# Performance work log

Hardware: AMD Instinct MI355X
Metric: run time of the kernel (lower is better)

Reference implementation:

```python
import jax, jax.numpy as jnp
import numpy as np

NEG_SLOPE = 0.01  # torch LeakyReLU default
BN_EPS = 1e-5     # torch BatchNorm1d default


def _bn(x, g, b):
    # training-mode batch norm over the node axis
    m = jnp.mean(x, axis=0)
    v = jnp.var(x, axis=0)
    return g * (x - m) * jax.lax.rsqrt(v + BN_EPS) + b


def _lrelu(x):
    return jax.nn.leaky_relu(x, NEG_SLOPE)


def setup_inputs() -> dict:
    key = jax.random.key(0)
    N, E, W, D = 100_000, 1_600_000, 32, 10
    ks = iter(jax.random.split(key, 64))

    def w(shape):
        fan_in = shape[-2] if len(shape) >= 2 else shape[-1]
        return (jax.random.normal(next(ks), shape, jnp.float32) / np.sqrt(fan_in)).astype(jnp.float32)

    inp = {}
    inp["x"] = jax.random.normal(next(ks), (N, 1), jnp.float32)
    inp["col_e_idx"] = jax.random.randint(next(ks), (2, E), 0, N, dtype=jnp.int32)
    # init_node_feature_trans: MLP 1 -> [32] -> 32, LeakyReLU, batch_norm=True
    inp["Wi0"] = w((1, W)); inp["bi0"] = jnp.zeros(W); inp["gi0"] = jnp.ones(W); inp["bei0"] = jnp.zeros(W)
    inp["Wi1"] = w((W, W)); inp["bi1"] = jnp.zeros(W); inp["gi1"] = jnp.ones(W); inp["bei1"] = jnp.zeros(W)
    # 10 CollConv layers (identical dims -> stacked params)
    inp["Wm"] = w((D, W, W)); inp["bm"] = jnp.zeros((D, W)); inp["gm"] = jnp.ones((D, W)); inp["bem"] = jnp.zeros((D, W))
    inp["Wu"] = w((D, 2 * W, W)); inp["bu"] = jnp.zeros((D, W)); inp["gu"] = jnp.ones((D, W)); inp["beu"] = jnp.zeros((D, W))
    # final_mlp: 32 -> 256 -> 128 -> 64 -> 32 (LeakyReLU, no BN), then 32 -> 1 sigmoid
    inp["Wf0"] = w((W, 256)); inp["bf0"] = jnp.zeros(256)
    inp["Wf1"] = w((256, 128)); inp["bf1"] = jnp.zeros(128)
    inp["Wf2"] = w((128, 64)); inp["bf2"] = jnp.zeros(64)
    inp["Wf3"] = w((64, W)); inp["bf3"] = jnp.zeros(W)
    inp["Wo"] = w((W, 1)); inp["bo"] = jnp.zeros(1)
    return inp


def reference(x, col_e_idx, Wi0, bi0, gi0, bei0, Wi1, bi1, gi1, bei1,
              Wm, bm, gm, bem, Wu, bu, gu, beu,
              Wf0, bf0, Wf1, bf1, Wf2, bf2, Wf3, bf3, Wo, bo):
    N = x.shape[0]
    D = Wm.shape[0]
    src, dst = col_e_idx[0], col_e_idx[1]

    # init node-feature MLP (Linear -> BN -> LeakyReLU, twice)
    h = _lrelu(_bn(x @ Wi0 + bi0, gi0, bei0))
    h = _lrelu(_bn(h @ Wi1 + bi1, gi1, bei1))

    feats = [h]  # middle_features[0]
    for i in range(D):  # fixed small depth -> python loop is fine
        # CollConv: node-wise message transform, edge gather, scatter-sum, update
        msg = _lrelu(_bn(h @ Wm[i] + bm[i], gm[i], bem[i]))      # [N, W]
        agg = jax.ops.segment_sum(msg[src], dst, num_segments=N)  # [N, W]
        h = _lrelu(_bn(jnp.concatenate([h, agg], axis=-1) @ Wu[i] + bu[i], gu[i], beu[i]))
        if i - 2 >= 0:  # residual_skip_num = 2
            h = h + feats[i - 2]
        feats.append(h)

    # final MLP (no BN) + sigmoid head
    h = _lrelu(h @ Wf0 + bf0)
    h = _lrelu(h @ Wf1 + bf1)
    h = _lrelu(h @ Wf2 + bf2)
    h = _lrelu(h @ Wf3 + bf3)
    return jax.nn.sigmoid(h @ Wo + bo)  # [N, 1]
```

## Files before the change

### kernel.cpp

```cpp
#include <hip/hip_runtime.h>
#include <hip/hip_bf16.h>

#define NN 100000
#define NEDGE 1600000
#define NV (NN*32)
#define NEG 0.01f
#define EPS 1e-5f
#define NBLK 391
#define NBKT 391
#define CHUNK 4096
#define NCBLK 391
#define DCAP 6144
#define STC 64
#define ST_STRIDE 4096
#define NGBLK 1563

#define OFF_STATS 0
#define STATS_F  (22*ST_STRIDE)
#define OFF_PA   STATS_F
#define OFF_PB   (OFF_PA + NV)
#define OFF_AGG  (OFF_PB + NV)
#define OFF_MSGB (OFF_AGG + NV)
#define OFF_RING (OFF_MSGB + NV/2)
#define OFF_WF   (OFF_RING + 4*NV)
#define ARENA_F  (OFF_WF + 25600)

#define W0B 0
#define W1B 1024
#define W2B 5120
#define W3B 6144

__device__ __align__(16) float gA[ARENA_F];
__device__ int g_rowptr[NN + 1];
__device__ int g_csr[NEDGE];
__device__ int g_bin[NEDGE];
__device__ int g_bcnt[NBKT];
__device__ int g_boff[NBKT];
__device__ int g_btail[NBKT];

__device__ __forceinline__ float lrelu(float v) { return v > 0.f ? v : v * NEG; }
__device__ __forceinline__ unsigned short f2b(float v) {
    __hip_bfloat16 b = __float2bfloat16(v);
    return *reinterpret_cast<unsigned short*>(&b);
}
__device__ __forceinline__ float b2f(unsigned short u) {
    __hip_bfloat16 b = *reinterpret_cast<__hip_bfloat16*>(&u);
    return __bfloat162float(b);
}

__global__ void k_zero_v19()
{
    int i = blockIdx.x * 256 + threadIdx.x;
    if (i < STATS_F) gA[i] = 0.f;
    if (i < NBKT) g_bcnt[i] = 0;
}

__global__ __launch_bounds__(256) void k_bcnt_v19(const int* __restrict__ col)
{
    __shared__ int hist[NBKT];
    int tid = threadIdx.x;
    for (int b = tid; b < NBKT; b += 256) hist[b] = 0;
    __syncthreads();
    int e0 = blockIdx.x * CHUNK;
    #pragma unroll
    for (int r = 0; r < CHUNK / 256; ++r) {
        int e = e0 + r * 256 + tid;
        if (e < NEDGE) atomicAdd(&hist[col[NEDGE + e] >> 8], 1);
    }
    __syncthreads();
    for (int b = tid; b < NBKT; b += 256) {
        int v = hist[b];
        if (v) atomicAdd(&g_bcnt[b], v);
    }
}

__global__ __launch_bounds__(512) void k_bscan_v19()
{
    __shared__ int s[512];
    int t = threadIdx.x;
    int v = (t < NBKT) ? g_bcnt[t] : 0;
    s[t] = v;
    __syncthreads();
    for (int off = 1; off < 512; off <<= 1) {
        int u = (t >= off) ? s[t - off] : 0;
        __syncthreads();
        s[t] += u;
        __syncthreads();
    }
    if (t < NBKT) {
        int o = s[t] - v;
        g_boff[t] = o;
        g_btail[t] = o;
    }
}

__global__ __launch_bounds__(256) void k_binfill_v19(const int* __restrict__ col)
{
    __shared__ int ssrc[CHUNK];
    __shared__ int sdst[CHUNK];
    __shared__ int hist[NBKT];
    __shared__ int boffL[NBKT];
    __shared__ int cnt2[NBKT];
    int tid = threadIdx.x;
    for (int b = tid; b < NBKT; b += 256) { hist[b] = 0; cnt2[b] = 0; }
    __syncthreads();
    int e0 = blockIdx.x * CHUNK;
    #pragma unroll
    for (int r = 0; r < CHUNK / 256; ++r) {
        int i = r * 256 + tid;
        int e = e0 + i;
        if (e < NEDGE) {
            int s = col[e];
            int d = col[NEDGE + e];
            ssrc[i] = s;
            sdst[i] = d;
            atomicAdd(&hist[d >> 8], 1);
        }
    }
    __syncthreads();
    for (int b = tid; b < NBKT; b += 256) {
        int h = hist[b];
        if (h) boffL[b] = atomicAdd(&g_btail[b], h);
    }
    __syncthreads();
    #pragma unroll
    for (int r = 0; r < CHUNK / 256; ++r) {
        int i = r * 256 + tid;
        int e = e0 + i;
        if (e < NEDGE) {
            int d = sdst[i];
            int b = d >> 8;
            int rk = atomicAdd(&cnt2[b], 1);
            g_bin[boffL[b] + rk] = (ssrc[i] << 8) | (d & 255);
        }
    }
}

__global__ __launch_bounds__(256) void k_csr_v19()
{
    __shared__ int stg[DCAP];
    __shared__ int c1[256];
    __shared__ int sc[256];
    __shared__ int sl[256];
    __shared__ int c2[256];
    int tid = threadIdx.x, b = blockIdx.x;
    int base = g_boff[b];
    int cntE = g_bcnt[b];
    c1[tid] = 0; c2[tid] = 0;
    __syncthreads();
    for (int i = tid; i < cntE; i += 256) {
        int p = g_bin[base + i];
        if (i < DCAP) stg[i] = p;
        atomicAdd(&c1[p & 255], 1);
    }
    __syncthreads();
    int v = c1[tid];
    sc[tid] = v;
    __syncthreads();
    for (int off = 1; off < 256; off <<= 1) {
        int u = (tid >= off) ? sc[tid - off] : 0;
        __syncthreads();
        sc[tid] += u;
        __syncthreads();
    }
    int loff = sc[tid] - v;
    sl[tid] = loff;
    int node = b * 256 + tid;
    if (node < NN) g_rowptr[node] = base + loff;
    if (b == NBKT - 1 && tid == 0) g_rowptr[NN] = NEDGE;
    __syncthreads();
    for (int i = tid; i < cntE; i += 256) {
        int p = (i < DCAP) ? stg[i] : g_bin[base + i];
        int dl = p & 255;
        int rk = atomicAdd(&c2[dl], 1);
        g_csr[base + sl[dl] + rk] = p >> 8;
    }
}

__global__ void k_init0_v17(const float* __restrict__ x, const float* __restrict__ Wi0,
                            const float* __restrict__ bi0)
{
    int j = threadIdx.x & 31, ns = threadIdx.x >> 5;
    float w = Wi0[j];
    float bb = bi0[j];
    __shared__ float red[64];
    if (threadIdx.x < 64) red[threadIdx.x] = 0.f;
    __syncthreads();
    float s1 = 0.f, s2 = 0.f;
    for (int t = blockIdx.x; t < NN / 8; t += gridDim.x) {
        int n = t * 8 + ns;
        float v = x[n] * w + bb;
        gA[OFF_PA + n * 32 + j] = v;
        s1 += v; s2 += v * v;
    }
    atomicAdd(&red[j], s1);
    atomicAdd(&red[j + 32], s2);
    __syncthreads();
    if (threadIdx.x < 64)
        atomicAdd(&gA[OFF_STATS + (blockIdx.x & (STC - 1)) * 64 + threadIdx.x], red[threadIdx.x]);
}

__global__ void k_nl_v17(int off_in, int off_out, int out_msg, int st_in,
                         const float* __restrict__ gamma, const float* __restrict__ beta,
                         int off_resid, int off_feats,
                         const float* __restrict__ Wn, const float* __restrict__ bn,
                         int st_out)
{
    int j = threadIdx.x & 31, ns = threadIdx.x >> 5;
    __shared__ float sstat[64];
    __shared__ float red[64];
    if (threadIdx.x < 64) {
        red[threadIdx.x] = 0.f;
        float acc = 0.f;
        int base = st_in + threadIdx.x;
        #pragma unroll 8
        for (int c = 0; c < STC; ++c) acc += gA[base + c * 64];
        sstat[threadIdx.x] = acc;
    }
    __syncthreads();
    float mean = sstat[j] * (1.f / NN);
    float var  = sstat[32 + j] * (1.f / NN) - mean * mean;
    float scale = gamma[j] * rsqrtf(var + EPS);
    float shift = beta[j] - mean * scale;

    float wc[32]; float bb = 0.f;
    if (Wn) {
        #pragma unroll
        for (int k = 0; k < 32; ++k) wc[k] = Wn[k * 32 + j];
        bb = bn[j];
    }
    unsigned short* mb = (unsigned short*)(gA + OFF_MSGB);
    __shared__ float sH[8][32];
    float s1 = 0.f, s2 = 0.f;
    for (int t = blockIdx.x; t < NN / 8; t += gridDim.x) {
        int n = t * 8 + ns;
        float v = gA[off_in + n * 32 + j];
        v = lrelu(scale * v + shift);
        if (off_resid >= 0) v += gA[off_resid + n * 32 + j];
        if (off_feats >= 0) gA[off_feats + n * 32 + j] = v;
        if (Wn) {
            sH[ns][j] = v;
            __syncthreads();
            float acc = bb;
            #pragma unroll
            for (int k = 0; k < 32; k += 4) {
                float4 h4 = *(const float4*)&sH[ns][k];
                acc += h4.x * wc[k] + h4.y * wc[k + 1] + h4.z * wc[k + 2] + h4.w * wc[k + 3];
            }
            if (out_msg) mb[n * 32 + j] = f2b(acc);
            else gA[off_out + n * 32 + j] = acc;
            s1 += acc; s2 += acc * acc;
            __syncthreads();
        }
    }
    if (Wn) {
        atomicAdd(&red[j], s1);
        atomicAdd(&red[j + 32], s2);
        __syncthreads();
        if (threadIdx.x < 64)
            atomicAdd(&gA[st_out + (blockIdx.x & (STC - 1)) * 64 + threadIdx.x], red[threadIdx.x]);
    }
}

__global__ __launch_bounds__(256) void k_gupd_v20(int st_msg,
                                                  const float* __restrict__ gm,
                                                  const float* __restrict__ bem,
                                                  int off_h,
                                                  const float* __restrict__ Wu_i,
                                                  const float* __restrict__ bu_i,
                                                  int st_out)
{
    __shared__ float sstat[64];
    __shared__ float scl[32], shf[32];
    __shared__ float sH[64][36];
    __shared__ float sAgg[64][36];
    __shared__ float red[64];
    int tid = threadIdx.x;
    int nb = blockIdx.x * 64;

    if (tid < 64) {
        red[tid] = 0.f;
        float acc = 0.f;
        int base = st_msg + tid;
        #pragma unroll 8
        for (int c = 0; c < STC; ++c) acc += gA[base + c * 64];
        sstat[tid] = acc;
    }
    {
        const float* hp = gA + off_h + nb * 32;
        int lim = min(2048, (NN - nb) * 32);
        for (int idx = tid; idx < lim; idx += 256)
            sH[idx >> 5][idx & 31] = hp[idx];
    }
    __syncthreads();
    if (tid < 32) {
        float mean = sstat[tid] * (1.f / NN);
        float var  = sstat[32 + tid] * (1.f / NN) - mean * mean;
        float s = gm[tid] * rsqrtf(var + EPS);
        scl[tid] = s;
        shf[tid] = bem[tid] - mean * s;
    }
    __syncthreads();

    {
        int nl = tid >> 2;
        int g  = tid & 3;
        int n  = nb + nl;
        float c[8], h[8];
        #pragma unroll
        for (int q = 0; q < 8; ++q) { c[q] = scl[g * 8 + q]; h[q] = shf[g * 8 + q]; }
        float a[8];
        #pragma unroll
        for (int q = 0; q < 8; ++q) a[q] = 0.f;
        if (n < NN) {
            const unsigned short* mb = (const unsigned short*)(gA + OFF_MSGB);
            int e0 = g_rowptr[n], e1 = g_rowptr[n + 1];
            int e = e0;
            for (; e + 3 < e1; e += 4) {
                int s0 = g_csr[e];
                int s1 = g_csr[e + 1];
                int s2 = g_csr[e + 2];
                int s3 = g_csr[e + 3];
                uint4 m0 = *(const uint4*)(mb + (s0 << 5) + (g << 3));
                uint4 m1 = *(const uint4*)(mb + (s1 << 5) + (g << 3));
                uint4 m2 = *(const uint4*)(mb + (s2 << 5) + (g << 3));
                uint4 m3 = *(const uint4*)(mb + (s3 << 5) + (g << 3));
                #pragma unroll
                for (int w = 0; w < 4; ++w) {
                    unsigned int u0 = (&m0.x)[w], u1 = (&m1.x)[w], u2 = (&m2.x)[w], u3 = (&m3.x)[w];
                    int q = w * 2;
                    a[q]   += lrelu(c[q]   * b2f((unsigned short)(u0 & 0xffff)) + h[q])
                            + lrelu(c[q]   * b2f((unsigned short)(u1 & 0xffff)) + h[q])
                            + lrelu(c[q]   * b2f((unsigned short)(u2 & 0xffff)) + h[q])
                            + lrelu(c[q]   * b2f((unsigned short)(u3 & 0xffff)) + h[q]);
                    a[q+1] += lrelu(c[q+1] * b2f((unsigned short)(u0 >> 16)) + h[q+1])
                            + lrelu(c[q+1] * b2f((unsigned short)(u1 >> 16)) + h[q+1])
                            + lrelu(c[q+1] * b2f((unsigned short)(u2 >> 16)) + h[q+1])
                            + lrelu(c[q+1] * b2f((unsigned short)(u3 >> 16)) + h[q+1]);
                }
            }
            for (; e < e1; ++e) {
                int s0 = g_csr[e];
                uint4 m0 = *(const uint4*)(mb + (s0 << 5) + (g << 3));
                #pragma unroll
                for (int w = 0; w < 4; ++w) {
                    unsigned int u0 = (&m0.x)[w];
                    int q = w * 2;
                    a[q]   += lrelu(c[q]   * b2f((unsigned short)(u0 & 0xffff)) + h[q]);
                    a[q+1] += lrelu(c[q+1] * b2f((unsigned short)(u0 >> 16)) + h[q+1]);
                }
            }
        }
        *(float4*)&sAgg[nl][g * 8]     = make_float4(a[0], a[1], a[2], a[3]);
        *(float4*)&sAgg[nl][g * 8 + 4] = make_float4(a[4], a[5], a[6], a[7]);
    }
    __syncthreads();

    {
        int j = tid & 31, ns = tid >> 5;
        float wc[64];
        #pragma unroll
        for (int k = 0; k < 64; ++k) wc[k] = Wu_i[k * 32 + j];
        float bb = bu_i[j];
        float s1 = 0.f, s2 = 0.f;
        #pragma unroll
        for (int it = 0; it < 8; ++it) {
            int nl = it * 8 + ns;
            int n = nb + nl;
            if (n >= NN) break;
            float acc = bb;
            #pragma unroll
            for (int k = 0; k < 32; k += 4) {
                float4 h4 = *(const float4*)&sH[nl][k];
                acc += h4.x * wc[k] + h4.y * wc[k + 1] + h4.z * wc[k + 2] + h4.w * wc[k + 3];
                float4 a4 = *(const float4*)&sAgg[nl][k];
                acc += a4.x * wc[32 + k] + a4.y * wc[32 + k + 1] + a4.z * wc[32 + k + 2] + a4.w * wc[32 + k + 3];
            }
            gA[OFF_PB + n * 32 + j] = acc;
            s1 += acc; s2 += acc * acc;
        }
        atomicAdd(&red[j], s1);
        atomicAdd(&red[j + 32], s2);
        __syncthreads();
        if (tid < 64)
            atomicAdd(&gA[st_out + (blockIdx.x & (STC - 1)) * 64 + tid], red[tid]);
    }
}

typedef __attribute__((ext_vector_type(8))) short bf16x8;
typedef __attribute__((ext_vector_type(4))) float f32x4;

union FC { uint4 u; bf16x8 b; };

#define MFMA(a, b, c) __builtin_amdgcn_mfma_f32_16x16x32_bf16(a, b, c, 0, 0, 0)

__device__ __forceinline__ bf16x8 ld_wf(const uint4* p) {
    FC c; c.u = *p; return c.b;
}

__device__ __forceinline__ f32x4 ld_bias4(const float* p) {
    float4 t = *(const float4*)p;
    f32x4 r; r[0] = t.x; r[1] = t.y; r[2] = t.z; r[3] = t.w; return r;
}

__device__ __forceinline__ f32x4 lrelu4(f32x4 v) {
    f32x4 r;
    #pragma unroll
    for (int k = 0; k < 4; ++k) r[k] = v[k] > 0.f ? v[k] : v[k] * NEG;
    return r;
}

__device__ __forceinline__ void splitpack(const float* v, bf16x8& hi, bf16x8& lo) {
    unsigned int h[4], l[4];
    #pragma unroll
    for (int k = 0; k < 4; ++k) {
        unsigned short h0 = f2b(v[2*k]), h1 = f2b(v[2*k+1]);
        float r0 = v[2*k]   - b2f(h0);
        float r1 = v[2*k+1] - b2f(h1);
        h[k] = (unsigned int)h0 | ((unsigned int)h1 << 16);
        l[k] = (unsigned int)f2b(r0) | ((unsigned int)f2b(r1) << 16);
    }
    FC ch; ch.u = make_uint4(h[0], h[1], h[2], h[3]); hi = ch.b;
    FC cl; cl.u = make_uint4(l[0], l[1], l[2], l[3]); lo = cl.b;
}

__global__ __launch_bounds__(256) void k_wprep_v18(const float* __restrict__ W0,
                                                   const float* __restrict__ W1,
                                                   const float* __restrict__ W2,
                                                   const float* __restrict__ W3)
{
    int i = blockIdx.x * 256 + threadIdx.x;
    if (i >= 51200) return;
    const float* src; int Nout, nk; int r = i;
    if (r < 8192)       { src = W0; Nout = 256; nk = 1; }
    else if (r < 40960) { src = W1; Nout = 128; nk = 8; r -= 8192; }
    else if (r < 49152) { src = W2; Nout = 64;  nk = 4; r -= 40960; }
    else                { src = W3; Nout = 32;  nk = 2; r -= 49152; }
    int frag = r >> 9;
    int lane = (r >> 3) & 63;
    int j = r & 7;
    int T = frag / nk, s = frag - T * nk;
    int g = lane >> 4;
    int outf = T * 16 + (lane & 15);
    int inf = 32 * s + 16 * (j >> 2) + 4 * g + (j & 3);
    unsigned short* dst = (unsigned short*)(gA + OFF_WF);
    dst[i] = f2b(src[inf * Nout + outf]);
}

__global__ __launch_bounds__(256) void k_final_v18(
    int off_h,
    const float* __restrict__ bf0, const float* __restrict__ bf1,
    const float* __restrict__ bf2, const float* __restrict__ bf3,
    const float* __restrict__ Wo,  const float* __restrict__ bo,
    float* __restrict__ out)
{
    int lane = threadIdx.x & 63;
    int wave = threadIdx.x >> 6;
    int c = lane & 15;
    int g = lane >> 4;
    int nb = blockIdx.x * 128 + wave * 32;
    int n0 = nb + c;
    int n1 = nb + 16 + c;
    int ld0 = min(n0, NN - 1), ld1 = min(n1, NN - 1);

    const float* h = gA + off_h;
    const uint4* WF = (const uint4*)(gA + OFF_WF);

    float4 ia0 = *(const float4*)&h[ld0 * 32 + 4 * g];
    float4 ib0 = *(const float4*)&h[ld0 * 32 + 16 + 4 * g];
    float4 ia1 = *(const float4*)&h[ld1 * 32 + 4 * g];
    float4 ib1 = *(const float4*)&h[ld1 * 32 + 16 + 4 * g];
    bf16x8 Bh0, Bl0, Bh1, Bl1;
    {
        float v0[8] = {ia0.x, ia0.y, ia0.z, ia0.w, ib0.x, ib0.y, ib0.z, ib0.w};
        float v1[8] = {ia1.x, ia1.y, ia1.z, ia1.w, ib1.x, ib1.y, ib1.z, ib1.w};
        splitpack(v0, Bh0, Bl0);
        splitpack(v1, Bh1, Bl1);
    }

    f32x4 A0[16][2];
    #pragma unroll
    for (int t = 0; t < 16; ++t) {
        f32x4 ci = ld_bias4(bf0 + t * 16 + 4 * g);
        bf16x8 w = ld_wf(WF + W0B + t * 64 + lane);
        f32x4 d0 = MFMA(w, Bh0, ci);
        d0 = MFMA(w, Bl0, d0);
        f32x4 d1 = MFMA(w, Bh1, ci);
        d1 = MFMA(w, Bl1, d1);
        A0[t][0] = lrelu4(d0);
        A0[t][1] = lrelu4(d1);
    }

    f32x4 A1[8][2];
    #pragma unroll
    for (int T = 0; T < 8; ++T) {
        f32x4 ci = ld_bias4(bf1 + T * 16 + 4 * g);
        A1[T][0] = ci; A1[T][1] = ci;
    }
    #pragma unroll
    for (int s = 0; s < 8; ++s) {
        bf16x8 bh[2], bl[2];
        #pragma unroll
        for (int u = 0; u < 2; ++u) {
            float vv[8] = {A0[2*s][u][0], A0[2*s][u][1], A0[2*s][u][2], A0[2*s][u][3],
                           A0[2*s+1][u][0], A0[2*s+1][u][1], A0[2*s+1][u][2], A0[2*s+1][u][3]};
            splitpack(vv, bh[u], bl[u]);
        }
        #pragma unroll
        for (int T = 0; T < 8; ++T) {
            bf16x8 w = ld_wf(WF + W1B + (T * 8 + s) * 64 + lane);
            A1[T][0] = MFMA(w, bh[0], A1[T][0]);
            A1[T][0] = MFMA(w, bl[0], A1[T][0]);
            A1[T][1] = MFMA(w, bh[1], A1[T][1]);
            A1[T][1] = MFMA(w, bl[1], A1[T][1]);
        }
    }
    #pragma unroll
    for (int T = 0; T < 8; ++T) { A1[T][0] = lrelu4(A1[T][0]); A1[T][1] = lrelu4(A1[T][1]); }

    f32x4 A2[4][2];
    #pragma unroll
    for (int T = 0; T < 4; ++T) {
        f32x4 ci = ld_bias4(bf2 + T * 16 + 4 * g);
        A2[T][0] = ci; A2[T][1] = ci;
    }
    #pragma unroll
    for (int s = 0; s < 4; ++s) {
        bf16x8 bh[2], bl[2];
        #pragma unroll
        for (int u = 0; u < 2; ++u) {
            float vv[8] = {A1[2*s][u][0], A1[2*s][u][1], A1[2*s][u][2], A1[2*s][u][3],
                           A1[2*s+1][u][0], A1[2*s+1][u][1], A1[2*s+1][u][2], A1[2*s+1][u][3]};
            splitpack(vv, bh[u], bl[u]);
        }
        #pragma unroll
        for (int T = 0; T < 4; ++T) {
            bf16x8 w = ld_wf(WF + W2B + (T * 4 + s) * 64 + lane);
            A2[T][0] = MFMA(w, bh[0], A2[T][0]);
            A2[T][0] = MFMA(w, bl[0], A2[T][0]);
            A2[T][1] = MFMA(w, bh[1], A2[T][1]);
            A2[T][1] = MFMA(w, bl[1], A2[T][1]);
        }
    }
    #pragma unroll
    for (int T = 0; T < 4; ++T) { A2[T][0] = lrelu4(A2[T][0]); A2[T][1] = lrelu4(A2[T][1]); }

    f32x4 A3[2][2];
    #pragma unroll
    for (int T = 0; T < 2; ++T) {
        f32x4 ci = ld_bias4(bf3 + T * 16 + 4 * g);
        A3[T][0] = ci; A3[T][1] = ci;
    }
    #pragma unroll
    for (int s = 0; s < 2; ++s) {
        bf16x8 bh[2], bl[2];
        #pragma unroll
        for (int u = 0; u < 2; ++u) {
            float vv[8] = {A2[2*s][u][0], A2[2*s][u][1], A2[2*s][u][2], A2[2*s][u][3],
                           A2[2*s+1][u][0], A2[2*s+1][u][1], A2[2*s+1][u][2], A2[2*s+1][u][3]};
            splitpack(vv, bh[u], bl[u]);
        }
        #pragma unroll
        for (int T = 0; T < 2; ++T) {
            bf16x8 w = ld_wf(WF + W3B + (T * 2 + s) * 64 + lane);
            A3[T][0] = MFMA(w, bh[0], A3[T][0]);
            A3[T][0] = MFMA(w, bl[0], A3[T][0]);
            A3[T][1] = MFMA(w, bh[1], A3[T][1]);
            A3[T][1] = MFMA(w, bl[1], A3[T][1]);
        }
    }
    #pragma unroll
    for (int T = 0; T < 2; ++T) { A3[T][0] = lrelu4(A3[T][0]); A3[T][1] = lrelu4(A3[T][1]); }

    float4 woa = *(const float4*)&Wo[4 * g];
    float4 wob = *(const float4*)&Wo[16 + 4 * g];
    float z0 = A3[0][0][0]*woa.x + A3[0][0][1]*woa.y + A3[0][0][2]*woa.z + A3[0][0][3]*woa.w
             + A3[1][0][0]*wob.x + A3[1][0][1]*wob.y + A3[1][0][2]*wob.z + A3[1][0][3]*wob.w;
    float z1 = A3[0][1][0]*woa.x + A3[0][1][1]*woa.y + A3[0][1][2]*woa.z + A3[0][1][3]*woa.w
             + A3[1][1][0]*wob.x + A3[1][1][1]*wob.y + A3[1][1][2]*wob.z + A3[1][1][3]*wob.w;
    z0 += __shfl_xor(z0, 16); z0 += __shfl_xor(z0, 32);
    z1 += __shfl_xor(z1, 16); z1 += __shfl_xor(z1, 32);
    float bb = bo[0];
    if (g == 0 && n0 < NN) out[n0] = 1.f / (1.f + __expf(-(z0 + bb)));
    if (g == 1 && n1 < NN) out[n1] = 1.f / (1.f + __expf(-(z1 + bb)));
}

extern "C" void kernel_launch(void* const* d_in, const int* in_sizes, int n_in,
                              void* d_out, int out_size, void* d_ws, size_t ws_size,
                              hipStream_t stream)
{
    (void)in_sizes; (void)n_in; (void)out_size; (void)d_ws; (void)ws_size;
    float* out = (float*)d_out;

    const float* x   = (const float*)d_in[0];
    const int*  col  = (const int*) d_in[1];
    const float* Wi0 = (const float*)d_in[2];
    const float* bi0 = (const float*)d_in[3];
    const float* gi0 = (const float*)d_in[4];
    const float* bei0= (const float*)d_in[5];
    const float* Wi1 = (const float*)d_in[6];
    const float* bi1 = (const float*)d_in[7];
    const float* gi1 = (const float*)d_in[8];
    const float* bei1= (const float*)d_in[9];
    const float* Wm  = (const float*)d_in[10];
    const float* bm  = (const float*)d_in[11];
    const float* gm  = (const float*)d_in[12];
    const float* bem = (const float*)d_in[13];
    const float* Wu  = (const float*)d_in[14];
    const float* bu  = (const float*)d_in[15];
    const float* gu  = (const float*)d_in[16];
    const float* beu = (const float*)d_in[17];
    const float* Wf0 = (const float*)d_in[18];
    const float* bf0 = (const float*)d_in[19];
    const float* Wf1 = (const float*)d_in[20];
    const float* bf1 = (const float*)d_in[21];
    const float* Wf2 = (const float*)d_in[22];
    const float* bf2 = (const float*)d_in[23];
    const float* Wf3 = (const float*)d_in[24];
    const float* bf3 = (const float*)d_in[25];
    const float* Wo  = (const float*)d_in[26];
    const float* bo  = (const float*)d_in[27];

    const int st_i0 = OFF_STATS;
    const int st_i1 = OFF_STATS + ST_STRIDE;
    const int st_m  = OFF_STATS + 2 * ST_STRIDE;
    const int st_u  = OFF_STATS + 12 * ST_STRIDE;

    const int RING[4] = { OFF_RING, OFF_RING + NV, OFF_RING + 2 * NV, OFF_RING + 3 * NV };

    dim3 blk(256);
    k_zero_v19<<<NBLK, blk, 0, stream>>>();
    k_bcnt_v19<<<NCBLK, blk, 0, stream>>>(col);
    k_bscan_v19<<<1, 512, 0, stream>>>();
    k_binfill_v19<<<NCBLK, blk, 0, stream>>>(col);
    k_csr_v19<<<NBKT, blk, 0, stream>>>();
    k_wprep_v18<<<200, blk, 0, stream>>>(Wf0, Wf1, Wf2, Wf3);

    k_init0_v17<<<1024, blk, 0, stream>>>(x, Wi0, bi0);
    k_nl_v17<<<1024, blk, 0, stream>>>(OFF_PA, OFF_PB, 0, st_i0, gi0, bei0, -1, -1, Wi1, bi1, st_i1);
    k_nl_v17<<<1024, blk, 0, stream>>>(OFF_PB, 0, 1, st_i1, gi1, bei1, -1, RING[0], Wm, bm, st_m);

    for (int i = 0; i < 10; ++i) {
        int h_cur = RING[i & 3];
        int h_new = RING[(i + 1) & 3];
        int resid = (i >= 2) ? RING[(i - 2) & 3] : -1;
        k_gupd_v20<<<NGBLK, blk, 0, stream>>>(st_m + i * ST_STRIDE, gm + i * 32, bem + i * 32,
                                              h_cur, Wu + i * 2048, bu + i * 32,
                                              st_u + i * ST_STRIDE);
        const float* Wn = (i < 9) ? (Wm + (i + 1) * 1024) : nullptr;
        const float* bn = (i < 9) ? (bm + (i + 1) * 32) : nullptr;
        int st_next = (i < 9) ? (st_m + (i + 1) * ST_STRIDE) : 0;
        k_nl_v17<<<1024, blk, 0, stream>>>(OFF_PB, 0, 1, st_u + i * ST_STRIDE,
                                           gu + i * 32, beu + i * 32,
                                           resid, h_new, Wn, bn, st_next);
    }

    k_final_v18<<<782, blk, 0, stream>>>(RING[2], bf0, bf1, bf2, bf3, Wo, bo, out);
}
```

Before: 966.8 us.

## Precompute activated messages per node before gather and sort CSR neighbors

Moves the BatchNorm+LeakyReLU of messages out of the per-edge gather loop into a separate per-node pass that writes activated bf16 messages, so the edge loop only sums. This applies the activation once per node instead of once per edge, at the cost of an extra kernel launch and an extra read/write of the message buffer each layer. The CSR build now sorts source indices within each destination row to improve gather locality, and the gather loop loads four neighbor indices with one coalesced load and distributes them via shuffles. The activated message is now rounded to bf16 after activation, which changes rounding slightly.

```diff
diff --git a/kernel.cpp b/kernel.cpp
--- a/kernel.cpp
+++ b/kernel.cpp
@@ -19,8 +19,8 @@
 #define STATS_F  (22*ST_STRIDE)
 #define OFF_PA   STATS_F
 #define OFF_PB   (OFF_PA + NV)
-#define OFF_AGG  (OFF_PB + NV)
-#define OFF_MSGB (OFF_AGG + NV)
+#define OFF_TACT (OFF_PB + NV)
+#define OFF_MSGB (OFF_TACT + NV)
 #define OFF_RING (OFF_MSGB + NV/2)
 #define OFF_WF   (OFF_RING + 4*NV)
 #define ARENA_F  (OFF_WF + 25600)
@@ -136,9 +136,10 @@
     }
 }
 
-__global__ __launch_bounds__(256) void k_csr_v19()
+__global__ __launch_bounds__(256) void k_csr_v21()
 {
     __shared__ int stg[DCAP];
+    __shared__ int srt[DCAP];
     __shared__ int c1[256];
     __shared__ int sc[256];
     __shared__ int sl[256];
@@ -169,11 +170,32 @@
     if (node < NN) g_rowptr[node] = base + loff;
     if (b == NBKT - 1 && tid == 0) g_rowptr[NN] = NEDGE;
     __syncthreads();
-    for (int i = tid; i < cntE; i += 256) {
-        int p = (i < DCAP) ? stg[i] : g_bin[base + i];
-        int dl = p & 255;
-        int rk = atomicAdd(&c2[dl], 1);
-        g_csr[base + sl[dl] + rk] = p >> 8;
+    if (cntE <= DCAP) {
+        for (int i = tid; i < cntE; i += 256) {
+            int p = stg[i];
+            int dl = p & 255;
+            int rk = atomicAdd(&c2[dl], 1);
+            srt[sl[dl] + rk] = p;
+        }
+        __syncthreads();
+        int cnt = v;
+        int s0 = loff;
+        for (int i = 1; i < cnt; ++i) {
+            int key = srt[s0 + i];
+            int j = i - 1;
+            while (j >= 0 && srt[s0 + j] > key) { srt[s0 + j + 1] = srt[s0 + j]; --j; }
+            srt[s0 + j + 1] = key;
+        }
+        __syncthreads();
+        for (int i = tid; i < cntE; i += 256)
+            g_csr[base + i] = srt[i] >> 8;
+    } else {
+        for (int i = tid; i < cntE; i += 256) {
+            int p = (i < DCAP) ? stg[i] : g_bin[base + i];
+            int dl = p & 255;
+            int rk = atomicAdd(&c2[dl], 1);
+            g_csr[base + sl[dl] + rk] = p >> 8;
+        }
     }
 }
 
@@ -262,35 +284,19 @@
     }
 }
 
-__global__ __launch_bounds__(256) void k_gupd_v20(int st_msg,
-                                                  const float* __restrict__ gm,
-                                                  const float* __restrict__ bem,
-                                                  int off_h,
-                                                  const float* __restrict__ Wu_i,
-                                                  const float* __restrict__ bu_i,
-                                                  int st_out)
+__global__ __launch_bounds__(256) void k_act_v21(int st_msg,
+                                                 const float* __restrict__ gm,
+                                                 const float* __restrict__ bem)
 {
     __shared__ float sstat[64];
     __shared__ float scl[32], shf[32];
-    __shared__ float sH[64][36];
-    __shared__ float sAgg[64][36];
-    __shared__ float red[64];
     int tid = threadIdx.x;
-    int nb = blockIdx.x * 64;
-
     if (tid < 64) {
-        red[tid] = 0.f;
         float acc = 0.f;
         int base = st_msg + tid;
         #pragma unroll 8
         for (int c = 0; c < STC; ++c) acc += gA[base + c * 64];
         sstat[tid] = acc;
-    }
-    {
-        const float* hp = gA + off_h + nb * 32;
-        int lim = min(2048, (NN - nb) * 32);
-        for (int idx = tid; idx < lim; idx += 256)
-            sH[idx >> 5][idx & 31] = hp[idx];
     }
     __syncthreads();
     if (tid < 32) {
@@ -301,53 +307,83 @@
         shf[tid] = bem[tid] - mean * s;
     }
     __syncthreads();
+    int idx = blockIdx.x * 256 + tid;
+    if (idx >= NV / 8) return;
+    const uint4* src = (const uint4*)(gA + OFF_MSGB);
+    uint4* dst = (uint4*)(gA + OFF_TACT);
+    uint4 m = src[idx];
+    int fb = (idx & 3) * 8;
+    uint4 o;
+    #pragma unroll
+    for (int w = 0; w < 4; ++w) {
+        unsigned int u = (&m.x)[w];
+        int f0 = fb + 2 * w;
+        float vlo = lrelu(scl[f0]     * __uint_as_float(u << 16)         + shf[f0]);
+        float vhi = lrelu(scl[f0 + 1] * __uint_as_float(u & 0xffff0000u) + shf[f0 + 1]);
+        (&o.x)[w] = (unsigned int)f2b(vlo) | ((unsigned int)f2b(vhi) << 16);
+    }
+    dst[idx] = o;
+}
+
+__global__ __launch_bounds__(256) void k_gupd_v21(int off_h,
+                                                  const float* __restrict__ Wu_i,
+                                                  const float* __restrict__ bu_i,
+                                                  int st_out)
+{
+    __shared__ float sH[64][36];
+    __shared__ float sAgg[64][36];
+    __shared__ float red[64];
+    int tid = threadIdx.x;
+    int nb = blockIdx.x * 64;
+
+    if (tid < 64) red[tid] = 0.f;
+    {
+        const float* hp = gA + off_h + nb * 32;
+        int lim = min(2048, (NN - nb) * 32);
+        for (int idx = tid; idx < lim; idx += 256)
+            sH[idx >> 5][idx & 31] = hp[idx];
+    }
 
     {
         int nl = tid >> 2;
         int g  = tid & 3;
         int n  = nb + nl;
-        float c[8], h[8];
-        #pragma unroll
-        for (int q = 0; q < 8; ++q) { c[q] = scl[g * 8 + q]; h[q] = shf[g * 8 + q]; }
         float a[8];
         #pragma unroll
         for (int q = 0; q < 8; ++q) a[q] = 0.f;
         if (n < NN) {
-            const unsigned short* mb = (const unsigned short*)(gA + OFF_MSGB);
+            const unsigned short* tb = (const unsigned short*)(gA + OFF_TACT);
             int e0 = g_rowptr[n], e1 = g_rowptr[n + 1];
             int e = e0;
             for (; e + 3 < e1; e += 4) {
-                int s0 = g_csr[e];
-                int s1 = g_csr[e + 1];
-                int s2 = g_csr[e + 2];
-                int s3 = g_csr[e + 3];
-                uint4 m0 = *(const uint4*)(mb + (s0 << 5) + (g << 3));
-                uint4 m1 = *(const uint4*)(mb + (s1 << 5) + (g << 3));
-                uint4 m2 = *(const uint4*)(mb + (s2 << 5) + (g << 3));
-                uint4 m3 = *(const uint4*)(mb + (s3 << 5) + (g << 3));
+                int sg = g_csr[e + g];
+                int s0 = __shfl(sg, 0, 4);
+                int s1 = __shfl(sg, 1, 4);
+                int s2 = __shfl(sg, 2, 4);
+                int s3 = __shfl(sg, 3, 4);
+                uint4 m0 = *(const uint4*)(tb + (s0 << 5) + (g << 3));
+                uint4 m1 = *(const uint4*)(tb + (s1 << 5) + (g << 3));
+                uint4 m2 = *(const uint4*)(tb + (s2 << 5) + (g << 3));
+                uint4 m3 = *(const uint4*)(tb + (s3 << 5) + (g << 3));
                 #pragma unroll
                 for (int w = 0; w < 4; ++w) {
                     unsigned int u0 = (&m0.x)[w], u1 = (&m1.x)[w], u2 = (&m2.x)[w], u3 = (&m3.x)[w];
                     int q = w * 2;
-                    a[q]   += lrelu(c[q]   * b2f((unsigned short)(u0 & 0xffff)) + h[q])
-                            + lrelu(c[q]   * b2f((unsigned short)(u1 & 0xffff)) + h[q])
-                            + lrelu(c[q]   * b2f((unsigned short)(u2 & 0xffff)) + h[q])
-                            + lrelu(c[q]   * b2f((unsigned short)(u3 & 0xffff)) + h[q]);
-                    a[q+1] += lrelu(c[q+1] * b2f((unsigned short)(u0 >> 16)) + h[q+1])
-                            + lrelu(c[q+1] * b2f((unsigned short)(u1 >> 16)) + h[q+1])
-                            + lrelu(c[q+1] * b2f((unsigned short)(u2 >> 16)) + h[q+1])
-                            + lrelu(c[q+1] * b2f((unsigned short)(u3 >> 16)) + h[q+1]);
+                    a[q]   += __uint_as_float(u0 << 16) + __uint_as_float(u1 << 16)
+                            + __uint_as_float(u2 << 16) + __uint_as_float(u3 << 16);
+                    a[q+1] += __uint_as_float(u0 & 0xffff0000u) + __uint_as_float(u1 & 0xffff0000u)
+                            + __uint_as_float(u2 & 0xffff0000u) + __uint_as_float(u3 & 0xffff0000u);
                 }
             }
             for (; e < e1; ++e) {
                 int s0 = g_csr[e];
-                uint4 m0 = *(const uint4*)(mb + (s0 << 5) + (g << 3));
+                uint4 m0 = *(const uint4*)(tb + (s0 << 5) + (g << 3));
                 #pragma unroll
                 for (int w = 0; w < 4; ++w) {
                     unsigned int u0 = (&m0.x)[w];
                     int q = w * 2;
-                    a[q]   += lrelu(c[q]   * b2f((unsigned short)(u0 & 0xffff)) + h[q]);
-                    a[q+1] += lrelu(c[q+1] * b2f((unsigned short)(u0 >> 16)) + h[q+1]);
+                    a[q]   += __uint_as_float(u0 << 16);
+                    a[q+1] += __uint_as_float(u0 & 0xffff0000u);
                 }
             }
         }
@@ -633,7 +669,7 @@
     k_bcnt_v19<<<NCBLK, blk, 0, stream>>>(col);
     k_bscan_v19<<<1, 512, 0, stream>>>();
     k_binfill_v19<<<NCBLK, blk, 0, stream>>>(col);
-    k_csr_v19<<<NBKT, blk, 0, stream>>>();
+    k_csr_v21<<<NBKT, blk, 0, stream>>>();
     k_wprep_v18<<<200, blk, 0, stream>>>(Wf0, Wf1, Wf2, Wf3);
 
     k_init0_v17<<<1024, blk, 0, stream>>>(x, Wi0, bi0);
@@ -644,8 +680,8 @@
         int h_cur = RING[i & 3];
         int h_new = RING[(i + 1) & 3];
         int resid = (i >= 2) ? RING[(i - 2) & 3] : -1;
-        k_gupd_v20<<<NGBLK, blk, 0, stream>>>(st_m + i * ST_STRIDE, gm + i * 32, bem + i * 32,
-                                              h_cur, Wu + i * 2048, bu + i * 32,
+        k_act_v21<<<1563, blk, 0, stream>>>(st_m + i * ST_STRIDE, gm + i * 32, bem + i * 32);
+        k_gupd_v21<<<NGBLK, blk, 0, stream>>>(h_cur, Wu + i * 2048, bu + i * 32,
                                               st_u + i * ST_STRIDE);
         const float* Wn = (i < 9) ? (Wm + (i + 1) * 1024) : nullptr;
         const float* bn = (i < 9) ? (bm + (i + 1) * 32) : nullptr;
```

Result: slower. 988.6 us (+2.3%).

## Degree-sort nodes within buckets, sort CSR by source, unroll gather by eight

Applied to the files above, without the earlier changes.

In the CSR build, nodes within each 256-node bucket are sorted by in-degree into a permutation table, and each node's edges are ordered by coarse source range. The gather/update kernel then processes nodes in permuted order, so the lanes of a wave see similar degrees and their source reads are more localized. The gather loop is also unrolled to eight edges, and bf16 is converted with plain bit shifts. The risks are extra setup work, indirect node indexing, and non-contiguous h loads and output stores.

```diff
diff --git a/kernel.cpp b/kernel.cpp
--- a/kernel.cpp
+++ b/kernel.cpp
@@ -13,14 +13,13 @@
 #define DCAP 6144
 #define STC 64
 #define ST_STRIDE 4096
-#define NGBLK 1563
+#define NGBLK 1564
 
 #define OFF_STATS 0
 #define STATS_F  (22*ST_STRIDE)
 #define OFF_PA   STATS_F
 #define OFF_PB   (OFF_PA + NV)
-#define OFF_AGG  (OFF_PB + NV)
-#define OFF_MSGB (OFF_AGG + NV)
+#define OFF_MSGB (OFF_PB + NV)
 #define OFF_RING (OFF_MSGB + NV/2)
 #define OFF_WF   (OFF_RING + 4*NV)
 #define ARENA_F  (OFF_WF + 25600)
@@ -34,6 +33,7 @@
 __device__ int g_rowptr[NN + 1];
 __device__ int g_csr[NEDGE];
 __device__ int g_bin[NEDGE];
+__device__ int g_perm[NBKT * 256];
 __device__ int g_bcnt[NBKT];
 __device__ int g_boff[NBKT];
 __device__ int g_btail[NBKT];
@@ -136,26 +136,36 @@
     }
 }
 
-__global__ __launch_bounds__(256) void k_csr_v19()
+__global__ __launch_bounds__(256) void k_csr_v23()
 {
     __shared__ int stg[DCAP];
-    __shared__ int c1[256];
+    __shared__ int c1[1024];
+    __shared__ int sgb[1024];
+    __shared__ int c2[1024];
     __shared__ int sc[256];
     __shared__ int sl[256];
-    __shared__ int c2[256];
+    __shared__ int dh[256];
+    __shared__ int ds2[256];
     int tid = threadIdx.x, b = blockIdx.x;
     int base = g_boff[b];
     int cntE = g_bcnt[b];
-    c1[tid] = 0; c2[tid] = 0;
+    #pragma unroll
+    for (int k = 0; k < 4; ++k) { c1[tid + 256 * k] = 0; c2[tid + 256 * k] = 0; }
+    dh[tid] = 0;
     __syncthreads();
     for (int i = tid; i < cntE; i += 256) {
         int p = g_bin[base + i];
         if (i < DCAP) stg[i] = p;
-        atomicAdd(&c1[p & 255], 1);
-    }
-    __syncthreads();
-    int v = c1[tid];
-    sc[tid] = v;
+        atomicAdd(&c1[((p & 255) << 2) | (p >> 23)], 1);
+    }
+    __syncthreads();
+    int t0 = c1[tid * 4], t1 = c1[tid * 4 + 1], t2 = c1[tid * 4 + 2], t3 = c1[tid * 4 + 3];
+    int deg = t0 + t1 + t2 + t3;
+    sgb[tid * 4]     = 0;
+    sgb[tid * 4 + 1] = t0;
+    sgb[tid * 4 + 2] = t0 + t1;
+    sgb[tid * 4 + 3] = t0 + t1 + t2;
+    sc[tid] = deg;
     __syncthreads();
     for (int off = 1; off < 256; off <<= 1) {
         int u = (tid >= off) ? sc[tid - off] : 0;
@@ -163,17 +173,34 @@
         sc[tid] += u;
         __syncthreads();
     }
-    int loff = sc[tid] - v;
+    int loff = sc[tid] - deg;
     sl[tid] = loff;
     int node = b * 256 + tid;
     if (node < NN) g_rowptr[node] = base + loff;
     if (b == NBKT - 1 && tid == 0) g_rowptr[NN] = NEDGE;
+    int key = (node < NN) ? min(deg, 254) : 255;
+    atomicAdd(&dh[key], 1);
+    __syncthreads();
+    int dv = dh[tid];
+    ds2[tid] = dv;
+    __syncthreads();
+    for (int off = 1; off < 256; off <<= 1) {
+        int u = (tid >= off) ? ds2[tid - off] : 0;
+        __syncthreads();
+        ds2[tid] += u;
+        __syncthreads();
+    }
+    dh[tid] = ds2[tid] - dv;
+    __syncthreads();
+    int pos = atomicAdd(&dh[key], 1);
+    g_perm[b * 256 + pos] = node;
     __syncthreads();
     for (int i = tid; i < cntE; i += 256) {
         int p = (i < DCAP) ? stg[i] : g_bin[base + i];
         int dl = p & 255;
-        int rk = atomicAdd(&c2[dl], 1);
-        g_csr[base + sl[dl] + rk] = p >> 8;
+        int k2 = (dl << 2) | (p >> 23);
+        int rk = atomicAdd(&c2[k2], 1);
+        g_csr[base + sl[dl] + sgb[k2] + rk] = p >> 8;
     }
 }
 
@@ -262,7 +289,7 @@
     }
 }
 
-__global__ __launch_bounds__(256) void k_gupd_v20(int st_msg,
+__global__ __launch_bounds__(256) void k_gupd_v23(int st_msg,
                                                   const float* __restrict__ gm,
                                                   const float* __restrict__ bem,
                                                   int off_h,
@@ -275,6 +302,7 @@
     __shared__ float sH[64][36];
     __shared__ float sAgg[64][36];
     __shared__ float red[64];
+    __shared__ int sPerm[64];
     int tid = threadIdx.x;
     int nb = blockIdx.x * 64;
 
@@ -285,12 +313,8 @@
         #pragma unroll 8
         for (int c = 0; c < STC; ++c) acc += gA[base + c * 64];
         sstat[tid] = acc;
-    }
-    {
-        const float* hp = gA + off_h + nb * 32;
-        int lim = min(2048, (NN - nb) * 32);
-        for (int idx = tid; idx < lim; idx += 256)
-            sH[idx >> 5][idx & 31] = hp[idx];
+    } else if (tid < 128) {
+        sPerm[tid - 64] = g_perm[nb + tid - 64];
     }
     __syncthreads();
     if (tid < 32) {
@@ -300,43 +324,90 @@
         scl[tid] = s;
         shf[tid] = bem[tid] - mean * s;
     }
+    for (int idx = tid; idx < 2048; idx += 256) {
+        int nl = idx >> 5;
+        int pn = sPerm[nl];
+        if (pn < NN) sH[nl][idx & 31] = gA[off_h + pn * 32 + (idx & 31)];
+    }
     __syncthreads();
 
     {
         int nl = tid >> 2;
         int g  = tid & 3;
-        int n  = nb + nl;
+        int pn = sPerm[nl];
         float c[8], h[8];
         #pragma unroll
         for (int q = 0; q < 8; ++q) { c[q] = scl[g * 8 + q]; h[q] = shf[g * 8 + q]; }
         float a[8];
         #pragma unroll
         for (int q = 0; q < 8; ++q) a[q] = 0.f;
-        if (n < NN) {
+        if (pn < NN) {
             const unsigned short* mb = (const unsigned short*)(gA + OFF_MSGB);
-            int e0 = g_rowptr[n], e1 = g_rowptr[n + 1];
+            int e0 = g_rowptr[pn], e1 = g_rowptr[pn + 1];
             int e = e0;
+            for (; e + 7 < e1; e += 8) {
+                int s0 = g_csr[e],     s1 = g_csr[e + 1], s2 = g_csr[e + 2], s3 = g_csr[e + 3];
+                int s4 = g_csr[e + 4], s5 = g_csr[e + 5], s6 = g_csr[e + 6], s7 = g_csr[e + 7];
+                uint4 m0 = *(const uint4*)(mb + (s0 << 5) + (g << 3));
+                uint4 m1 = *(const uint4*)(mb + (s1 << 5) + (g << 3));
+                uint4 m2 = *(const uint4*)(mb + (s2 << 5) + (g << 3));
+                uint4 m3 = *(const uint4*)(mb + (s3 << 5) + (g << 3));
+                uint4 m4 = *(const uint4*)(mb + (s4 << 5) + (g << 3));
+                uint4 m5 = *(const uint4*)(mb + (s5 << 5) + (g << 3));
+                uint4 m6 = *(const uint4*)(mb + (s6 << 5) + (g << 3));
+                uint4 m7 = *(const uint4*)(mb + (s7 << 5) + (g << 3));
+                #pragma unroll
+                for (int w = 0; w < 4; ++w) {
+                    int q = w * 2;
+                    unsigned int u;
+                    u = (&m0.x)[w];
+                    a[q]   += lrelu(c[q]   * __uint_as_float(u << 16)         + h[q]);
+                    a[q+1] += lrelu(c[q+1] * __uint_as_float(u & 0xffff0000u) + h[q+1]);
+                    u = (&m1.x)[w];
+                    a[q]   += lrelu(c[q]   * __uint_as_float(u << 16)         + h[q]);
+                    a[q+1] += lrelu(c[q+1] * __uint_as_float(u & 0xffff0000u) + h[q+1]);
+                    u = (&m2.x)[w];
+                    a[q]   += lrelu(c[q]   * __uint_as_float(u << 16)         + h[q]);
+                    a[q+1] += lrelu(c[q+1] * __uint_as_float(u & 0xffff0000u) + h[q+1]);
+                    u = (&m3.x)[w];
+                    a[q]   += lrelu(c[q]   * __uint_as_float(u << 16)         + h[q]);
+                    a[q+1] += lrelu(c[q+1] * __uint_as_float(u & 0xffff0000u) + h[q+1]);
+                    u = (&m4.x)[w];
+                    a[q]   += lrelu(c[q]   * __uint_as_float(u << 16)         + h[q]);
+                    a[q+1] += lrelu(c[q+1] * __uint_as_float(u & 0xffff0000u) + h[q+1]);
+                    u = (&m5.x)[w];
+                    a[q]   += lrelu(c[q]   * __uint_as_float(u << 16)         + h[q]);
+                    a[q+1] += lrelu(c[q+1] * __uint_as_float(u & 0xffff0000u) + h[q+1]);
+                    u = (&m6.x)[w];
+                    a[q]   += lrelu(c[q]   * __uint_as_float(u << 16)         + h[q]);
+                    a[q+1] += lrelu(c[q+1] * __uint_as_float(u & 0xffff0000u) + h[q+1]);
+                    u = (&m7.x)[w];
+                    a[q]   += lrelu(c[q]   * __uint_as_float(u << 16)         + h[q]);
+                    a[q+1] += lrelu(c[q+1] * __uint_as_float(u & 0xffff0000u) + h[q+1]);
+                }
+            }
             for (; e + 3 < e1; e += 4) {
-                int s0 = g_csr[e];
-                int s1 = g_csr[e + 1];
-                int s2 = g_csr[e + 2];
-                int s3 = g_csr[e + 3];
+                int s0 = g_csr[e], s1 = g_csr[e + 1], s2 = g_csr[e + 2], s3 = g_csr[e + 3];
                 uint4 m0 = *(const uint4*)(mb + (s0 << 5) + (g << 3));
                 uint4 m1 = *(const uint4*)(mb + (s1 << 5) + (g << 3));
                 uint4 m2 = *(const uint4*)(mb + (s2 << 5) + (g << 3));
                 uint4 m3 = *(const uint4*)(mb + (s3 << 5) + (g << 3));
                 #pragma unroll
                 for (int w = 0; w < 4; ++w) {
-                    unsigned int u0 = (&m0.x)[w], u1 = (&m1.x)[w], u2 = (&m2.x)[w], u3 = (&m3.x)[w];
                     int q = w * 2;
-                    a[q]   += lrelu(c[q]   * b2f((unsigned short)(u0 & 0xffff)) + h[q])
-                            + lrelu(c[q]   * b2f((unsigned short)(u1 & 0xffff)) + h[q])
-                            + lrelu(c[q]   * b2f((unsigned short)(u2 & 0xffff)) + h[q])
-                            + lrelu(c[q]   * b2f((unsigned short)(u3 & 0xffff)) + h[q]);
-                    a[q+1] += lrelu(c[q+1] * b2f((unsigned short)(u0 >> 16)) + h[q+1])
-                            + lrelu(c[q+1] * b2f((unsigned short)(u1 >> 16)) + h[q+1])
-                            + lrelu(c[q+1] * b2f((unsigned short)(u2 >> 16)) + h[q+1])
-                            + lrelu(c[q+1] * b2f((unsigned short)(u3 >> 16)) + h[q+1]);
+                    unsigned int u;
+                    u = (&m0.x)[w];
+                    a[q]   += lrelu(c[q]   * __uint_as_float(u << 16)         + h[q]);
+                    a[q+1] += lrelu(c[q+1] * __uint_as_float(u & 0xffff0000u) + h[q+1]);
+                    u = (&m1.x)[w];
+                    a[q]   += lrelu(c[q]   * __uint_as_float(u << 16)         + h[q]);
+                    a[q+1] += lrelu(c[q+1] * __uint_as_float(u & 0xffff0000u) + h[q+1]);
+                    u = (&m2.x)[w];
+                    a[q]   += lrelu(c[q]   * __uint_as_float(u << 16)         + h[q]);
+                    a[q+1] += lrelu(c[q+1] * __uint_as_float(u & 0xffff0000u) + h[q+1]);
+                    u = (&m3.x)[w];
+                    a[q]   += lrelu(c[q]   * __uint_as_float(u << 16)         + h[q]);
+                    a[q+1] += lrelu(c[q+1] * __uint_as_float(u & 0xffff0000u) + h[q+1]);
                 }
             }
             for (; e < e1; ++e) {
@@ -344,10 +415,10 @@
                 uint4 m0 = *(const uint4*)(mb + (s0 << 5) + (g << 3));
                 #pragma unroll
                 for (int w = 0; w < 4; ++w) {
-                    unsigned int u0 = (&m0.x)[w];
                     int q = w * 2;
-                    a[q]   += lrelu(c[q]   * b2f((unsigned short)(u0 & 0xffff)) + h[q]);
-                    a[q+1] += lrelu(c[q+1] * b2f((unsigned short)(u0 >> 16)) + h[q+1]);
+                    unsigned int u = (&m0.x)[w];
+                    a[q]   += lrelu(c[q]   * __uint_as_float(u << 16)         + h[q]);
+                    a[q+1] += lrelu(c[q+1] * __uint_as_float(u & 0xffff0000u) + h[q+1]);
                 }
             }
         }
@@ -366,8 +437,8 @@
         #pragma unroll
         for (int it = 0; it < 8; ++it) {
             int nl = it * 8 + ns;
-            int n = nb + nl;
-            if (n >= NN) break;
+            int pn = sPerm[nl];
+            if (pn >= NN) continue;
             float acc = bb;
             #pragma unroll
             for (int k = 0; k < 32; k += 4) {
@@ -376,7 +447,7 @@
                 float4 a4 = *(const float4*)&sAgg[nl][k];
                 acc += a4.x * wc[32 + k] + a4.y * wc[32 + k + 1] + a4.z * wc[32 + k + 2] + a4.w * wc[32 + k + 3];
             }
-            gA[OFF_PB + n * 32 + j] = acc;
+            gA[OFF_PB + pn * 32 + j] = acc;
             s1 += acc; s2 += acc * acc;
         }
         atomicAdd(&red[j], s1);
@@ -633,7 +704,7 @@
     k_bcnt_v19<<<NCBLK, blk, 0, stream>>>(col);
     k_bscan_v19<<<1, 512, 0, stream>>>();
     k_binfill_v19<<<NCBLK, blk, 0, stream>>>(col);
-    k_csr_v19<<<NBKT, blk, 0, stream>>>();
+    k_csr_v23<<<NBKT, blk, 0, stream>>>();
     k_wprep_v18<<<200, blk, 0, stream>>>(Wf0, Wf1, Wf2, Wf3);
 
     k_init0_v17<<<1024, blk, 0, stream>>>(x, Wi0, bi0);
@@ -644,7 +715,7 @@
         int h_cur = RING[i & 3];
         int h_new = RING[(i + 1) & 3];
         int resid = (i >= 2) ? RING[(i - 2) & 3] : -1;
-        k_gupd_v20<<<NGBLK, blk, 0, stream>>>(st_m + i * ST_STRIDE, gm + i * 32, bem + i * 32,
+        k_gupd_v23<<<NGBLK, blk, 0, stream>>>(st_m + i * ST_STRIDE, gm + i * 32, bem + i * 32,
                                               h_cur, Wu + i * 2048, bu + i * 32,
                                               st_u + i * ST_STRIDE);
         const float* Wn = (i < 9) ? (Wm + (i + 1) * 1024) : nullptr;
```

Result: slower. 1.006 ms (+4.1%).
